# Performance work log

Measured on AMD Instinct MI355X. Metric: run time of the kernel, lower is better.

Reference implementation:

```python
import jax, jax.numpy as jnp
import numpy as np

B, S, N_CATE, N_CONT = 32, 1024, 4, 4
HIDDEN, ATTN, VOCAB, EMB = 1024, 512, 1000, 128


def sinusoidal_pe(seq_len, d_model, base=10000.0):
    pos = jnp.arange(seq_len, dtype=jnp.float32)[:, None]            # [S,1]
    i = jnp.arange(d_model // 2, dtype=jnp.float32)[None, :]         # [1,D/2]
    ang = pos / jnp.power(base, 2.0 * i / d_model)                   # [S,D/2]
    pe = jnp.zeros((seq_len, d_model), dtype=jnp.float32)
    pe = pe.at[:, 0::2].set(jnp.sin(ang))
    pe = pe.at[:, 1::2].set(jnp.cos(ang))
    return pe


def setup_inputs() -> dict:
    key = jax.random.key(0)
    ks = jax.random.split(key, 20)
    s = 0.02
    inp = {
        "cate_x": jax.random.randint(ks[0], (B, S, N_CATE), 0, VOCAB, dtype=jnp.int64)
                  if jax.config.read("jax_enable_x64") else
                  jax.random.randint(ks[0], (B, S, N_CATE), 0, VOCAB, dtype=jnp.int32),
        "cont_x": jax.random.normal(ks[1], (B, S, N_CONT), dtype=jnp.float32),
        "mask": jnp.ones((B, S), dtype=bool),
        "targets": jax.random.uniform(ks[2], (B, S), dtype=jnp.float32),
        # EntireEmbedding params: 4 cate tables + cont linear + comb projection
        "E0": jax.random.normal(ks[3], (VOCAB, EMB), dtype=jnp.float32) * s,
        "E1": jax.random.normal(ks[4], (VOCAB, EMB), dtype=jnp.float32) * s,
        "E2": jax.random.normal(ks[5], (VOCAB, EMB), dtype=jnp.float32) * s,
        "E3": jax.random.normal(ks[6], (VOCAB, EMB), dtype=jnp.float32) * s,
        "Wc": jax.random.normal(ks[7], (N_CONT, N_CATE * EMB), dtype=jnp.float32) * s,
        "Wproj": jax.random.normal(ks[8], (2 * N_CATE * EMB, HIDDEN), dtype=jnp.float32) * s,
        # two-head attention linears (bias=False)
        "WQ1": jax.random.normal(ks[9], (HIDDEN, ATTN), dtype=jnp.float32) * s,
        "WK1": jax.random.normal(ks[10], (HIDDEN, ATTN), dtype=jnp.float32) * s,
        "WV1": jax.random.normal(ks[11], (HIDDEN, ATTN), dtype=jnp.float32) * s,
        "WQ2": jax.random.normal(ks[12], (HIDDEN, ATTN), dtype=jnp.float32) * s,
        "WK2": jax.random.normal(ks[13], (HIDDEN, ATTN), dtype=jnp.float32) * s,
        "WV2": jax.random.normal(ks[14], (HIDDEN, ATTN), dtype=jnp.float32) * s,
        "W0": jax.random.normal(ks[15], (2 * ATTN, HIDDEN), dtype=jnp.float32) * s,
        "Wf": jax.random.normal(ks[16], (HIDDEN, 1), dtype=jnp.float32) * s,
    }
    return inp


def _attend(x, WQ, WK, WV):
    Q = x @ WQ  # [B,S,A]
    K = x @ WK
    V = x @ WV
    scores = jnp.einsum("bqd,bkd->bqk", Q, K) / jnp.sqrt(jnp.float32(ATTN))
    # faithful to nn.Softmax(dim=1): normalize over the QUERY axis
    attn = jax.nn.softmax(scores, axis=1)
    return jnp.einsum("bqk,bkv->bqv", attn, V)


def reference(cate_x, cont_x, mask, targets, E0, E1, E2, E3, Wc, Wproj,
              WQ1, WK1, WV1, WQ2, WK2, WV2, W0, Wf):
    # EntireEmbedding: per-feature cate embeddings + cont projection -> comb proj
    cate_emb = jnp.concatenate(
        [E0[cate_x[..., 0]], E1[cate_x[..., 1]], E2[cate_x[..., 2]], E3[cate_x[..., 3]]],
        axis=-1)                                   # [B,S,512]
    cont_emb = cont_x @ Wc                          # [B,S,512]
    x = jnp.concatenate([cate_emb, cont_emb], axis=-1) @ Wproj  # [B,S,H]
    x = x + sinusoidal_pe(x.shape[1], HIDDEN)[None, :, :]
    z1 = _attend(x, WQ1, WK1, WV1)                  # [B,S,A]
    z2 = _attend(x, WQ2, WK2, WV2)                  # [B,S,A]
    z = jnp.concatenate([z1, z2], axis=-1) @ W0     # [B,S,H]
    out = jax.nn.sigmoid(z @ Wf)                    # FinalConnecting: Linear(H,1)+sigmoid
    return out.squeeze(-1)                          # [B,S]
```

## Files before the change

kernel.cpp:

```cpp
#include <hip/hip_runtime.h>
#include <hip/hip_bf16.h>
#include <math.h>

#define BB    32
#define SS    1024
#define HID   1024
#define AT    512
#define NVOC  1000
#define NT    (BB*SS)

typedef unsigned short u16;
typedef __attribute__((ext_vector_type(8))) short s16x8;
typedef __attribute__((ext_vector_type(4))) float f32x4;

__device__ __forceinline__ float bf2f(u16 u) {
    union { unsigned int i; float f; } x; x.i = ((unsigned int)u) << 16; return x.f;
}
__device__ __forceinline__ u16 f2bf(float f) {
    union { float f; unsigned int i; } u; u.f = f;
    unsigned int r = u.i + 0x7fffu + ((u.i >> 16) & 1u);
    return (u16)(r >> 16);
}
__device__ __forceinline__ float4 ld4(const float* p) { return *(const float4*)p; }
__device__ __forceinline__ float4 ld4bf(const u16* p) {
    ushort4 v = *(const ushort4*)p;
    return make_float4(bf2f(v.x), bf2f(v.y), bf2f(v.z), bf2f(v.w));
}
__device__ __forceinline__ void unpack8(uint4 v, float* x) {
    x[0] = bf2f((u16)(v.x & 0xffff)); x[1] = bf2f((u16)(v.x >> 16));
    x[2] = bf2f((u16)(v.y & 0xffff)); x[3] = bf2f((u16)(v.y >> 16));
    x[4] = bf2f((u16)(v.z & 0xffff)); x[5] = bf2f((u16)(v.z >> 16));
    x[6] = bf2f((u16)(v.w & 0xffff)); x[7] = bf2f((u16)(v.w >> 16));
}

__device__ __forceinline__ void gld16(const u16* g, u16* l) {
    __builtin_amdgcn_global_load_lds(
        (const __attribute__((address_space(1))) unsigned int*)g,
        (__attribute__((address_space(3))) unsigned int*)l,
        16, 0, 0);
}

struct Ptrs4f { const float* p[4]; };

__device__ __forceinline__ float blockReduceSum(float x) {
    #pragma unroll
    for (int off = 32; off > 0; off >>= 1) x += __shfl_down(x, off, 64);
    __shared__ float tmp[4];
    int lane = threadIdx.x & 63, wid = threadIdx.x >> 6;
    if (lane == 0) tmp[wid] = x;
    __syncthreads();
    if (threadIdx.x == 0) x = tmp[0] + tmp[1] + tmp[2] + tmp[3];
    return x;
}
__device__ __forceinline__ float waveReduceSum(float x) {
    #pragma unroll
    for (int off = 32; off > 0; off >>= 1) x += __shfl_down(x, off, 64);
    return x;
}

__global__ void k_s1(Ptrs4f E, const float* __restrict__ Wproj, Ptrs4f W,
                     const float* __restrict__ W0, const float* __restrict__ Wf,
                     u16* __restrict__ PE16, u16* __restrict__ E16o, u16* __restrict__ Wp16,
                     u16* __restrict__ Wt, float* __restrict__ W0f,
                     float* __restrict__ Wcp, float* __restrict__ CQ) {
    int blk = blockIdx.x, tid = threadIdx.x;
    if (blk < 2048) {
        int idx = blk*256 + tid;
        int s = idx >> 9, i = idx & 511;
        const float l2_10000 = 13.287712379549449f;
        float denom = exp2f((2.f * (float)i / 1024.f) * l2_10000);
        float ang = (float)s / denom;
        unsigned int pack = ((unsigned int)f2bf(__cosf(ang)) << 16) | f2bf(__sinf(ang));
        *(unsigned int*)(PE16 + (size_t)s*1024 + 2*i) = pack;
    } else if (blk < 4048) {
        int id2 = blk - 2048;
        int f = id2 / 500;
        int i = (id2 % 500)*256 + tid;
        E16o[(size_t)f*128000 + i] = f2bf(E.p[f][i]);
    } else if (blk < 6096) {
        int i = (blk - 4048)*256 + tid;
        Wp16[i] = f2bf(Wproj[i]);
    } else if (blk < 8144) {
        int tb = blk - 6096;
        int mat = tb >> 9, t2 = tb & 511;
        int cx = t2 & 15, ry = t2 >> 4;
        int r0 = ry*32, c0 = cx*32;
        const float* in = W.p[mat];
        u16* out = Wt + (size_t)mat*1024*512;
        __shared__ float tt[32][33];
        int tx = tid & 31, ty8 = tid >> 5;
        #pragma unroll
        for (int it = 0; it < 4; ++it)
            tt[ty8 + it*8][tx] = in[(size_t)(r0 + ty8 + it*8)*512 + c0 + tx];
        __syncthreads();
        #pragma unroll
        for (int it = 0; it < 4; ++it)
            out[(size_t)(c0 + ty8 + it*8)*1024 + r0 + tx] = f2bf(tt[tx][ty8 + it*8]);
    } else if (blk < 8400) {
        int wave = tid >> 6, lane = tid & 63;
        int row = (blk - 8144)*4 + wave;
        const float* rp = W0 + (size_t)row*1024;
        float a = 0.f;
        #pragma unroll
        for (int i = 0; i < 16; ++i) {
            int j = i*64 + lane;
            a += rp[j] * Wf[j];
        }
        a = waveReduceSum(a);
        if (lane == 0) W0f[row] = a;
    } else {
        int idx = (blk - 8400)*256 + tid;
        if (idx < 4096) Wcp[idx] = 0.f;
        else CQ[idx - 4096] = 0.f;
    }
}

__global__ void k_s2(const float* __restrict__ Wc, const float* __restrict__ Wproj,
                     Ptrs4f W, const float* __restrict__ WV1, const float* __restrict__ WV2,
                     const float* __restrict__ W0f, float* __restrict__ Wcp, float* __restrict__ v) {
    int blk = blockIdx.x, tid = threadIdx.x;
    if (blk < 64) {
        int c = blk >> 4, ic = (blk >> 2) & 3, jc = blk & 3;
        int i = ic*256 + tid;
        float a = 0.f;
        for (int j = jc*128; j < jc*128 + 128; ++j)
            a += Wc[c*512 + j] * Wproj[(size_t)(512 + j)*1024 + i];
        atomicAdd(&Wcp[c*1024 + i], a);
    } else {
        int b2 = blk - 64;
        int h = b2 >> 10, i = b2 & 1023;
        const float* WV = h ? WV2 : WV1;
        const float* wf = W0f + h*512;
        float a = 0.f;
        for (int aa = tid; aa < 512; aa += 256) a += WV[(size_t)i*512 + aa] * wf[aa];
        a = blockReduceSum(a);
        if (tid == 0) v[h*1024 + i] = a;
    }
}

__device__ __forceinline__ void cstore(float* p, float v) { *p = v; }
__device__ __forceinline__ void cstore(u16* p, float v)   { *p = f2bf(v); }

template<typename CT, bool CTRANS>
__device__ __forceinline__ void mfma_gemm(const u16* __restrict__ A, const u16* __restrict__ B,
                                          CT* __restrict__ C, int M, int N, int K, float alpha,
                                          int m0, int n0) {
    __shared__ u16 As[128*64];
    __shared__ u16 Bs[128*64];
    const int tid = threadIdx.x;
    const int wave = tid >> 6, lane = tid & 63;
    const int quad = lane >> 4, l16 = lane & 15;
    const int wm = (wave >> 1)*64, wn = (wave & 1)*64;
    const int srow = lane >> 3;
    const int scol = ((lane & 7) ^ srow) * 8;
    f32x4 acc[4][4] = {};

    for (int k0 = 0; k0 < K; k0 += 64) {
        #pragma unroll
        for (int p = 0; p < 4; ++p) {
            int rb = wave*32 + p*8;
            gld16(A + (size_t)(m0 + rb + srow)*K + k0 + scol, As + rb*64);
            gld16(B + (size_t)(n0 + rb + srow)*K + k0 + scol, Bs + rb*64);
        }
        __syncthreads();
        #pragma unroll
        for (int kk = 0; kk < 2; ++kk) {
            s16x8 af[4], bf[4];
            #pragma unroll
            for (int i = 0; i < 4; ++i) {
                int row = wm + i*16 + l16;
                af[i] = *(const s16x8*)(As + row*64 + (((kk*4 + quad) ^ (row & 7)) * 8));
            }
            #pragma unroll
            for (int j = 0; j < 4; ++j) {
                int row = wn + j*16 + l16;
                bf[j] = *(const s16x8*)(Bs + row*64 + (((kk*4 + quad) ^ (row & 7)) * 8));
            }
            #pragma unroll
            for (int i = 0; i < 4; ++i)
                #pragma unroll
                for (int j = 0; j < 4; ++j)
                    acc[i][j] = __builtin_amdgcn_mfma_f32_16x16x32_bf16(af[i], bf[j], acc[i][j], 0, 0, 0);
        }
        __syncthreads();
    }
    #pragma unroll
    for (int i = 0; i < 4; ++i) {
        #pragma unroll
        for (int r = 0; r < 4; ++r) {
            int gm = m0 + wm + i*16 + quad*4 + r;
            if (gm < M) {
                #pragma unroll
                for (int j = 0; j < 4; ++j) {
                    int gn = n0 + wn + j*16 + l16;
                    if (CTRANS) cstore(C + (size_t)gn*M + gm, acc[i][j][r] * alpha);
                    else        cstore(C + (size_t)gm*N + gn, acc[i][j][r] * alpha);
                }
            }
        }
    }
}

__global__ __launch_bounds__(256) void k_s3(const u16* __restrict__ Wp16, const u16* __restrict__ Wt,
                                            u16* __restrict__ PWT,
                                            const u16* __restrict__ PE16, u16* __restrict__ PEQ16,
                                            Ptrs4f W, const float* __restrict__ Wcp, float* __restrict__ CQ,
                                            const float* __restrict__ Wproj, const float* __restrict__ v,
                                            float* __restrict__ pv) {
    int blk = blockIdx.x, tid = threadIdx.x;
    if (blk < 64) {
        int x = blk & 3, z = blk >> 2;
        int f = z >> 2, w = z & 3;
        mfma_gemm<u16,true>(Wp16 + (size_t)f*128*1024, Wt + (size_t)w*512*1024,
                            PWT + (size_t)z*512*128, 128, 512, 1024, 1.f, 0, x*128);
    } else if (blk < 192) {
        int idx = blk - 64;
        int w = idx >> 5, r2 = idx & 31, y = r2 >> 2, x = r2 & 3;
        mfma_gemm<u16,false>(PE16, Wt + (size_t)w*512*1024, PEQ16 + (size_t)w*1024*512,
                             1024, 512, 1024, 1.f, y*128, x*128);
    } else if (blk < 448) {
        int r = blk - 192;
        int ns = r & 1, wc = (r >> 1) & 15, jc = r >> 5;
        int w = wc & 3, c = wc >> 2; int n = ns*256 + tid;
        const float* Ww = W.p[w];
        float a = 0.f;
        for (int j = jc*128; j < jc*128 + 128; ++j) a += Wcp[c*1024 + j] * Ww[(size_t)j*512 + n];
        atomicAdd(&CQ[(size_t)(w*4 + c)*512 + n], a);
    } else {
        int b2 = blk - 448;
        int i = b2 & 127, fh = b2 >> 7; int f = fh >> 1, h = fh & 1;
        const float* row = Wproj + (size_t)(f*128 + i)*1024;
        const float* vh = v + h*1024;
        float a = 0.f;
        for (int j = tid; j < 1024; j += 256) a += row[j] * vh[j];
        a = blockReduceSum(a);
        if (tid == 0) pv[(size_t)fh*128 + i] = a;
    }
}

__global__ __launch_bounds__(256) void k_s4(const u16* __restrict__ E16, const u16* __restrict__ PWT,
                                            const u16* __restrict__ PE16,
                                            u16* __restrict__ TQK16,
                                            const float* __restrict__ Wcp, const float* __restrict__ v,
                                            const float* __restrict__ pv,
                                            float* __restrict__ Ut, float* __restrict__ pu, float* __restrict__ cu) {
    int blk = blockIdx.x, tid = threadIdx.x;
    int wave = tid >> 6, lane = tid & 63;
    if (blk < 512) {
        int z = blk >> 5, r = blk & 31, y = r >> 2, x = r & 3;
        int f = z >> 2;
        mfma_gemm<u16,false>(E16 + (size_t)f*128000, PWT + (size_t)z*512*128,
                   TQK16 + (size_t)z*1000*512, 1000, 512, 128, 1.f, y*128, x*128);
        return;
    }
    int id = blk - 512;
    if (id < 32) {
        int d = id*256 + tid;
        if (d < 8000) {
            int f = d / 2000, h = (d / 1000) & 1, r = d % 1000;
            const u16* er = E16 + ((size_t)f*1000 + r)*128;
            const float* pvp = pv + (size_t)(f*2 + h)*128;
            float a = 0.f;
            #pragma unroll
            for (int q = 0; q < 16; ++q) {
                float xv[8];
                unpack8(*(const uint4*)(er + q*8), xv);
                #pragma unroll
                for (int e = 0; e < 8; ++e) a += xv[e] * pvp[q*8 + e];
            }
            Ut[(size_t)(f*2 + h)*1000 + r] = a;
        }
    } else if (id < 544) {
        int d = (id - 32)*4 + wave;
        int h = d >> 10, s = d & 1023;
        float a = 0.f;
        #pragma unroll
        for (int half = 0; half < 2; ++half) {
            int k = half*512 + lane*8;
            float xv[8];
            unpack8(*(const uint4*)(PE16 + (size_t)s*1024 + k), xv);
            float4 b0 = ld4(v + h*1024 + k), b1 = ld4(v + h*1024 + k + 4);
            a += xv[0]*b0.x + xv[1]*b0.y + xv[2]*b0.z + xv[3]*b0.w
               + xv[4]*b1.x + xv[5]*b1.y + xv[6]*b1.z + xv[7]*b1.w;
        }
        a = waveReduceSum(a);
        if (lane == 0) pu[h*1024 + s] = a;
    } else {
        #pragma unroll
        for (int rep = 0; rep < 2; ++rep) {
            int d = wave*2 + rep;
            int h = d >> 2, c = d & 3;
            float a = 0.f;
            #pragma unroll
            for (int i = 0; i < 16; ++i) {
                int j = i*64 + lane;
                a += Wcp[c*1024 + j] * v[h*1024 + j];
            }
            a = waveReduceSum(a);
            if (lane == 0) cu[h*4 + c] = a;
        }
    }
}

__global__ __launch_bounds__(512, 2) void k_g_S256(
        const u16* __restrict__ Q, const u16* __restrict__ K,
        u16* __restrict__ Sb, float alpha,
        float* __restrict__ Pm, float* __restrict__ Pd, int b0) {
    __shared__ u16 As[2][16384];
    __shared__ u16 Bs[2][16384];
    const int tid = threadIdx.x;
    const int wave = tid >> 6, lane = tid & 63;
    const int quad = lane >> 4, l16 = lane & 15;
    const int wm = wave >> 2, wn = wave & 3;

    const int nwg = (int)gridDim.x;
    int fblk = (int)blockIdx.x;
    int qq = nwg >> 3, rr = nwg & 7;
    int xcd = fblk & 7, idx = fblk >> 3;
    int swz = (xcd < rr ? xcd*(qq + 1) : rr*(qq + 1) + (xcd - rr)*qq) + idx;
    int b = swz >> 4, tile = swz & 15;
    int m0 = (tile >> 2) << 8, n0 = (tile & 3) << 8;

    const u16* __restrict__ Ab = Q + (size_t)b*SS*AT;
    const u16* __restrict__ Bb = K + (size_t)b*SS*AT;
    u16* __restrict__ C = Sb + (size_t)b*SS*SS;

    const int srow = lane >> 3;
    const int scol = ((lane & 7) ^ srow) * 8;

    f32x4 acc[8][4] = {};

    auto stageA = [&](int kt, int q) {
        gld16(Ab + (size_t)(m0 + q*64 + wave*8 + srow)*AT + kt*64 + scol,
              &As[kt & 1][q*4096 + wave*512]);
    };
    auto stageB = [&](int kt, int q) {
        gld16(Bb + (size_t)(n0 + q*64 + wave*8 + srow)*AT + kt*64 + scol,
              &Bs[kt & 1][q*4096 + wave*512]);
    };

    s16x8 af[4][2];
    s16x8 bf[4][2];

    auto readA = [&](int c, int ih) {
        #pragma unroll
        for (int i2 = 0; i2 < 4; ++i2) {
            int row = wm*128 + (ih*4 + i2)*16 + l16;
            #pragma unroll
            for (int kk = 0; kk < 2; ++kk)
                af[i2][kk] = *(const s16x8*)(&As[c][row*64 + (((kk*4 + quad) ^ (row & 7)) * 8)]);
        }
    };
    auto readB2 = [&](int c, int jh) {
        #pragma unroll
        for (int j2 = 0; j2 < 2; ++j2) {
            int j = jh*2 + j2;
            int row = wn*64 + j*16 + l16;
            #pragma unroll
            for (int kk = 0; kk < 2; ++kk)
                bf[j][kk] = *(const s16x8*)(&Bs[c][row*64 + (((kk*4 + quad) ^ (row & 7)) * 8)]);
        }
    };
    auto mma16 = [&](int ih, int jh) {
        __builtin_amdgcn_s_setprio(1);
        #pragma unroll
        for (int i2 = 0; i2 < 4; ++i2)
            #pragma unroll
            for (int j2 = 0; j2 < 2; ++j2) {
                int i = ih*4 + i2, j = jh*2 + j2;
                acc[i][j] = __builtin_amdgcn_mfma_f32_16x16x32_bf16(af[i2][0], bf[j][0], acc[i][j], 0, 0, 0);
                acc[i][j] = __builtin_amdgcn_mfma_f32_16x16x32_bf16(af[i2][1], bf[j][1], acc[i][j], 0, 0, 0);
            }
        __builtin_amdgcn_s_setprio(0);
    };
    auto midsync = [&]() {
        __builtin_amdgcn_s_barrier();
        asm volatile("s_waitcnt lgkmcnt(0)" ::: "memory");
        __builtin_amdgcn_sched_barrier(0);
    };

    #pragma unroll
    for (int q = 0; q < 4; ++q) stageA(0, q);
    #pragma unroll
    for (int q = 0; q < 4; ++q) stageB(0, q);
    stageA(1, 0); stageA(1, 2);
    stageB(1, 0); stageB(1, 1); stageB(1, 2); stageB(1, 3);
    asm volatile("s_waitcnt vmcnt(6)" ::: "memory");
    __builtin_amdgcn_s_barrier();

    #pragma unroll
    for (int t = 0; t < 8; ++t) {
        const int c = t & 1;
        readA(c, 0);
        readB2(c, 0);
        if (t <= 6) { stageA(t + 1, 1); stageA(t + 1, 3); }
        midsync();
        mma16(0, 0);
        __builtin_amdgcn_s_barrier();
        readB2(c, 1);
        if (t <= 5) { stageA(t + 2, 0); stageA(t + 2, 2); }
        midsync();
        mma16(0, 1);
        __builtin_amdgcn_s_barrier();
        readA(c, 1);
        if (t <= 5) { stageB(t + 2, 0); stageB(t + 2, 1); }
        midsync();
        mma16(1, 0);
        __builtin_amdgcn_s_barrier();
        if (t <= 5) { stageB(t + 2, 2); stageB(t + 2, 3); }
        midsync();
        mma16(1, 1);
        if (t <= 5)      asm volatile("s_waitcnt vmcnt(6)" ::: "memory");
        else if (t == 6) asm volatile("s_waitcnt vmcnt(0)" ::: "memory");
        __builtin_amdgcn_sched_barrier(0);
        __builtin_amdgcn_s_barrier();
    }

    #pragma unroll
    for (int i = 0; i < 8; ++i) {
        #pragma unroll
        for (int r = 0; r < 4; ++r) {
            int gm = m0 + wm*128 + i*16 + quad*4 + r;
            u16 q0 = f2bf(acc[i][0][r] * alpha);
            u16 q1 = f2bf(acc[i][1][r] * alpha);
            u16 q2 = f2bf(acc[i][2][r] * alpha);
            u16 q3 = f2bf(acc[i][3][r] * alpha);
            acc[i][0][r] = bf2f(q0); acc[i][1][r] = bf2f(q1);
            acc[i][2][r] = bf2f(q2); acc[i][3][r] = bf2f(q3);
            unsigned int lo = (unsigned int)q0 | ((unsigned int)q1 << 16);
            unsigned int hi = (unsigned int)q2 | ((unsigned int)q3 << 16);
            *(uint2*)(C + (size_t)gm*SS + n0 + wn*64 + l16*4) = make_uint2(lo, hi);
        }
    }
    float* sM = (float*)&As[0][0];
    float* sS = (float*)&Bs[0][0];
    #pragma unroll
    for (int j = 0; j < 4; ++j) {
        float mx = -3.4e38f;
        #pragma unroll
        for (int i = 0; i < 8; ++i)
            #pragma unroll
            for (int r = 0; r < 4; ++r) mx = fmaxf(mx, acc[i][j][r]);
        mx = fmaxf(mx, __shfl_xor(mx, 16, 64));
        mx = fmaxf(mx, __shfl_xor(mx, 32, 64));
        float sm = 0.f;
        #pragma unroll
        for (int i = 0; i < 8; ++i)
            #pragma unroll
            for (int r = 0; r < 4; ++r) sm += exp2f(acc[i][j][r] - mx);
        sm += __shfl_xor(sm, 16, 64);
        sm += __shfl_xor(sm, 32, 64);
        if (quad == 0) { sM[wave*64 + j*16 + l16] = mx; sS[wave*64 + j*16 + l16] = sm; }
    }
    __syncthreads();
    if (tid < 256) {
        int c = tid, wq = c >> 6, cc = c & 63;
        float ma = sM[wq*64 + cc],       sa = sS[wq*64 + cc];
        float mb = sM[(4 + wq)*64 + cc], sb2 = sS[(4 + wq)*64 + cc];
        float mm = fmaxf(ma, mb);
        float ss = sa * exp2f(ma - mm) + sb2 * exp2f(mb - mm);
        size_t po = ((size_t)(b0 + b)*4 + (m0 >> 8))*1024;
        Pm[po + n0 + c] = mm;
        Pd[po + n0 + c] = ss;
    }
}

__global__ __launch_bounds__(256) void k_gather(
                         const int* __restrict__ cate, const float* __restrict__ cont,
                         const u16* __restrict__ TQK, const float* __restrict__ CQ,
                         const u16* __restrict__ PEQ, const float* __restrict__ Ut,
                         const float* __restrict__ cu, const float* __restrict__ pu,
                         u16* __restrict__ Qh, u16* __restrict__ Kh,
                         float* __restrict__ u, int h) {
    int tid = threadIdx.x;
    int g = blockIdx.x & 7;
    size_t t = (size_t)(blockIdx.x >> 3)*32 + (tid >> 3);
    int cslot = tid & 7;
    int s = (int)(t & 1023);
    int4 cc = *(const int4*)(cate + t*4);
    float4 cv = ld4(cont + t*4);
    int n = g*64 + cslot*8;
    #pragma unroll
    for (int e = 0; e < 2; ++e) {
        int w = 2*h + e;
        const u16* t0 = TQK + ((size_t)(0*4  + w)*1000 + cc.x)*512 + n;
        const u16* t1 = TQK + ((size_t)(1*4  + w)*1000 + cc.y)*512 + n;
        const u16* t2 = TQK + ((size_t)(2*4  + w)*1000 + cc.z)*512 + n;
        const u16* t3 = TQK + ((size_t)(3*4  + w)*1000 + cc.w)*512 + n;
        const u16* pq = PEQ + ((size_t)w*1024 + s)*512 + n;
        const float* cq = CQ + (size_t)w*2048 + n;
        float a0[8], a1[8], a2[8], a3[8], ap[8];
        unpack8(*(const uint4*)t0, a0); unpack8(*(const uint4*)t1, a1);
        unpack8(*(const uint4*)t2, a2); unpack8(*(const uint4*)t3, a3);
        unpack8(*(const uint4*)pq, ap);
        unsigned int pack[4];
        #pragma unroll
        for (int jp = 0; jp < 4; ++jp) {
            float x0, x1;
            #pragma unroll
            for (int half = 0; half < 2; ++half) {
                int j = jp*2 + half;
                float x = a0[j] + a1[j] + a2[j] + a3[j] + ap[j]
                        + cv.x*cq[j] + cv.y*cq[512+j] + cv.z*cq[1024+j] + cv.w*cq[1536+j];
                if (half == 0) x0 = x; else x1 = x;
            }
            pack[jp] = ((unsigned int)f2bf(x1) << 16) | f2bf(x0);
        }
        u16* op = (e ? Kh : Qh) + t*512 + n;
        *(uint4*)op = make_uint4(pack[0], pack[1], pack[2], pack[3]);
    }
    if (g == 0 && (tid & 7) == 0) {
        float uu = pu[h*1024 + s]
                 + Ut[(0*2 + h)*1000 + cc.x] + Ut[(1*2 + h)*1000 + cc.y]
                 + Ut[(2*2 + h)*1000 + cc.z] + Ut[(3*2 + h)*1000 + cc.w]
                 + cv.x*cu[h*4+0] + cv.y*cu[h*4+1] + cv.z*cu[h*4+2] + cv.w*cu[h*4+3];
        u[(size_t)h*NT + t] = uu;
    }
}

__global__ __launch_bounds__(1024) void k_logit(const u16* __restrict__ Sb,
                        const float* __restrict__ Pm, const float* __restrict__ Pd,
                        const float* __restrict__ u,
                        float* __restrict__ logits, float* __restrict__ out,
                        int b0, int mode) {
    __shared__ float wsm[1024];
    int wave = threadIdx.x >> 6, lane = threadIdx.x & 63;
    size_t bi = (size_t)(gridDim.x - 1 - blockIdx.x);
    size_t tl0 = bi*16;
    size_t tabs0 = (size_t)b0*1024 + tl0;
    int ab = (int)(tabs0 >> 10);
    {
        int k = threadIdx.x;
        float mx = -3.4e38f;
        #pragma unroll
        for (int mt = 0; mt < 4; ++mt) mx = fmaxf(mx, Pm[((size_t)ab*4 + mt)*1024 + k]);
        float dd = 0.f;
        #pragma unroll
        for (int mt = 0; mt < 4; ++mt) dd += Pd[((size_t)ab*4 + mt)*1024 + k]
                                           * exp2f(Pm[((size_t)ab*4 + mt)*1024 + k] - mx);
        int q = (k & ~63) | (((k & 15) << 2) | ((k & 63) >> 4));
        wsm[q] = u[(size_t)ab*1024 + k] / dd * exp2f(-mx);
    }
    __syncthreads();
    size_t tl = tl0 + wave;
    size_t tabs = tabs0 + wave;
    const u16* row = Sb + tl*1024;
    float acc = 0.f;
    #pragma unroll
    for (int half = 0; half < 2; ++half) {
        int k = lane*8 + half*512;
        float sv[8];
        unpack8(*(const uint4*)(row + k), sv);
        float4 w0 = ld4(wsm + k), w1 = ld4(wsm + k + 4);
        acc += exp2f(sv[0])*w0.x + exp2f(sv[1])*w0.y + exp2f(sv[2])*w0.z + exp2f(sv[3])*w0.w
             + exp2f(sv[4])*w1.x + exp2f(sv[5])*w1.y + exp2f(sv[6])*w1.z + exp2f(sv[7])*w1.w;
    }
    acc = waveReduceSum(acc);
    if (lane == 0) {
        if (mode == 0) logits[tabs] = acc;
        else {
            float x = logits[tabs] + acc;
            out[tabs] = 1.f / (1.f + expf(-x));
        }
    }
}

extern "C" void kernel_launch(void* const* d_in, const int* in_sizes, int n_in,
                              void* d_out, int out_size, void* d_ws, size_t ws_size,
                              hipStream_t stream) {
    const int*   cate = (const int*)d_in[0];
    const float* cont = (const float*)d_in[1];
    Ptrs4f E; E.p[0] = (const float*)d_in[4]; E.p[1] = (const float*)d_in[5];
              E.p[2] = (const float*)d_in[6]; E.p[3] = (const float*)d_in[7];
    const float* Wc    = (const float*)d_in[8];
    const float* Wproj = (const float*)d_in[9];
    Ptrs4f W; W.p[0] = (const float*)d_in[10];
              W.p[1] = (const float*)d_in[11];
              W.p[2] = (const float*)d_in[13];
              W.p[3] = (const float*)d_in[14];
    const float* WV1 = (const float*)d_in[12];
    const float* WV2 = (const float*)d_in[15];
    const float* W0  = (const float*)d_in[16];
    const float* Wf  = (const float*)d_in[17];

    char* base = (char*)d_ws;
    size_t off = 0;
    auto alloc = [&](size_t bytes) { void* p = base + off; off += (bytes + 255) & ~(size_t)255; return p; };
    u16*   PE16  = (u16*)  alloc(1048576ull*2);
    u16*   E16   = (u16*)  alloc(4ull*1000*128*2);
    u16*   Wt    = (u16*)  alloc(4ull*512*1024*2);
    u16*   Wp16  = (u16*)  alloc(512ull*1024*2);
    u16*   PWT   = (u16*)  alloc(16ull*512*128*2);
    u16*   TQK16 = (u16*)  alloc(16ull*1000*512*2);
    u16*   PEQ16 = (u16*)  alloc(4ull*1024*512*2);
    float* Wcp   = (float*)alloc(4*1024*4);
    float* W0f   = (float*)alloc(1024*4);
    float* vv    = (float*)alloc(2*1024*4);
    float* CQ    = (float*)alloc(16*512*4);
    float* pvb   = (float*)alloc(8*128*4);
    float* Ut    = (float*)alloc(8*1000*4);
    float* cu    = (float*)alloc(8*4);
    float* pu    = (float*)alloc(2*1024*4);
    float* ubuf  = (float*)alloc(2ull*NT*4);
    u16*   Qh    = (u16*)  alloc((size_t)NT*512*2);
    u16*   Kh    = (u16*)  alloc((size_t)NT*512*2);
    float* Pm    = (float*)alloc(32ull*8*1024*4);
    float* Pd    = (float*)alloc(32ull*8*1024*4);
    float* logits= (float*)alloc((size_t)NT*4);
    size_t sChunkBytes = (size_t)SS*SS*2;
    size_t remain = (ws_size > off) ? (ws_size - off) : 0;
    int NB = (int)(remain / sChunkBytes);
    if (NB > 32) NB = 32;
    if (NB < 1) NB = 1;
    u16* Sbuf = (u16*)(base + off);

    const float alpha = 0.06375954951107036f;

    k_s1<<<8448, 256, 0, stream>>>(E, Wproj, W, W0, Wf, PE16, E16, Wp16, Wt, W0f, Wcp, CQ);
    k_s2<<<2112, 256, 0, stream>>>(Wc, Wproj, W, WV1, WV2, W0f, Wcp, vv);
    k_s3<<<1472, 256, 0, stream>>>(Wp16, Wt, PWT, PE16, PEQ16, W, Wcp, CQ, Wproj, vv, pvb);
    k_s4<<<1057, 256, 0, stream>>>(E16, PWT, PE16, TQK16, Wcp, vv, pvb, Ut, pu, cu);

    for (int h = 0; h < 2; ++h) {
        k_gather<<<8192, 256, 0, stream>>>(cate, cont, TQK16, CQ, PEQ16, Ut, cu, pu, Qh, Kh, ubuf, h);
        for (int b0 = 0; b0 < 32; b0 += NB) {
            int nb = (32 - b0 < NB) ? (32 - b0) : NB;
            k_g_S256<<<16*nb, 512, 0, stream>>>(Qh + (size_t)b0*SS*AT, Kh + (size_t)b0*SS*AT,
                                                Sbuf, alpha, Pm, Pd, b0);
            k_logit<<<nb*64, 1024, 0, stream>>>(Sbuf, Pm, Pd, ubuf + (size_t)h*NT,
                                                logits, (float*)d_out, b0, h);
        }
    }
}
```

Baseline: 339.1 us.

## Compute two N-tiles per workgroup with continuous pipeline across tiles

Each QK^T GEMM workgroup now computes two adjacent 256x256 score tiles, running a single 16-step loop whose prefetch carries straight from the first tile into the second, with the epilogue (bf16 store plus column max/sum partials) emitted in the middle and at the end. This halves the grid and hides the pipeline ramp-up and drain of the second tile, at the cost of less parallelism (256 workgroups per chunk) and dedicated shared memory for the partials. Separately, k_logit's shared weight array is transposed to [8][128] so that lanes read consecutive addresses, avoiding bank conflicts from the float4 loads.

```diff
diff --git a/kernel.cpp b/kernel.cpp
--- a/kernel.cpp
+++ b/kernel.cpp
@@ -308,6 +308,8 @@
         float* __restrict__ Pm, float* __restrict__ Pd, int b0) {
     __shared__ u16 As[2][16384];
     __shared__ u16 Bs[2][16384];
+    __shared__ float sM[8][64];
+    __shared__ float sS[8][64];
     const int tid = threadIdx.x;
     const int wave = tid >> 6, lane = tid & 63;
     const int quad = lane >> 4, l16 = lane & 15;
@@ -318,8 +320,9 @@
     int qq = nwg >> 3, rr = nwg & 7;
     int xcd = fblk & 7, idx = fblk >> 3;
     int swz = (xcd < rr ? xcd*(qq + 1) : rr*(qq + 1) + (xcd - rr)*qq) + idx;
-    int b = swz >> 4, tile = swz & 15;
-    int m0 = (tile >> 2) << 8, n0 = (tile & 3) << 8;
+    int b = swz >> 3, tile = swz & 7;
+    int m0 = (tile >> 1) << 8;
+    int nbase = (tile & 1) << 9;
 
     const u16* __restrict__ Ab = Q + (size_t)b*SS*AT;
     const u16* __restrict__ Bb = K + (size_t)b*SS*AT;
@@ -330,13 +333,16 @@
 
     f32x4 acc[8][4] = {};
 
-    auto stageA = [&](int kt, int q) {
+    auto stageA = [&](int t, int q) {
+        int kt = t & 7;
         gld16(Ab + (size_t)(m0 + q*64 + wave*8 + srow)*AT + kt*64 + scol,
-              &As[kt & 1][q*4096 + wave*512]);
+              &As[t & 1][q*4096 + wave*512]);
     };
-    auto stageB = [&](int kt, int q) {
-        gld16(Bb + (size_t)(n0 + q*64 + wave*8 + srow)*AT + kt*64 + scol,
-              &Bs[kt & 1][q*4096 + wave*512]);
+    auto stageB = [&](int t, int q) {
+        int kt = t & 7;
+        int nn = nbase + ((t >> 3) << 8);
+        gld16(Bb + (size_t)(nn + q*64 + wave*8 + srow)*AT + kt*64 + scol,
+              &Bs[t & 1][q*4096 + wave*512]);
     };
 
     s16x8 af[4][2];
@@ -377,6 +383,55 @@
         __builtin_amdgcn_s_barrier();
         asm volatile("s_waitcnt lgkmcnt(0)" ::: "memory");
         __builtin_amdgcn_sched_barrier(0);
+    };
+
+    auto epilogue = [&](int half) {
+        int n0h = nbase + half*256;
+        #pragma unroll
+        for (int i = 0; i < 8; ++i) {
+            #pragma unroll
+            for (int r = 0; r < 4; ++r) {
+                int gm = m0 + wm*128 + i*16 + quad*4 + r;
+                u16 q0 = f2bf(acc[i][0][r] * alpha);
+                u16 q1 = f2bf(acc[i][1][r] * alpha);
+                u16 q2 = f2bf(acc[i][2][r] * alpha);
+                u16 q3 = f2bf(acc[i][3][r] * alpha);
+                acc[i][0][r] = bf2f(q0); acc[i][1][r] = bf2f(q1);
+                acc[i][2][r] = bf2f(q2); acc[i][3][r] = bf2f(q3);
+                unsigned int lo = (unsigned int)q0 | ((unsigned int)q1 << 16);
+                unsigned int hi = (unsigned int)q2 | ((unsigned int)q3 << 16);
+                *(uint2*)(C + (size_t)gm*SS + n0h + wn*64 + l16*4) = make_uint2(lo, hi);
+            }
+        }
+        #pragma unroll
+        for (int j = 0; j < 4; ++j) {
+            float mx = -3.4e38f;
+            #pragma unroll
+            for (int i = 0; i < 8; ++i)
+                #pragma unroll
+                for (int r = 0; r < 4; ++r) mx = fmaxf(mx, acc[i][j][r]);
+            mx = fmaxf(mx, __shfl_xor(mx, 16, 64));
+            mx = fmaxf(mx, __shfl_xor(mx, 32, 64));
+            float sm = 0.f;
+            #pragma unroll
+            for (int i = 0; i < 8; ++i)
+                #pragma unroll
+                for (int r = 0; r < 4; ++r) sm += exp2f(acc[i][j][r] - mx);
+            sm += __shfl_xor(sm, 16, 64);
+            sm += __shfl_xor(sm, 32, 64);
+            if (quad == 0) { sM[wave][j*16 + l16] = mx; sS[wave][j*16 + l16] = sm; }
+        }
+        __syncthreads();
+        if (tid < 256) {
+            int c = tid, wq = c >> 6, cc = c & 63;
+            float ma = sM[wq][cc],     sa = sS[wq][cc];
+            float mb = sM[4 + wq][cc], sb2 = sS[4 + wq][cc];
+            float mm = fmaxf(ma, mb);
+            float ss = sa * exp2f(ma - mm) + sb2 * exp2f(mb - mm);
+            size_t po = ((size_t)(b0 + b)*4 + (m0 >> 8))*1024;
+            Pm[po + n0h + c] = mm;
+            Pd[po + n0h + c] = ss;
+        }
     };
 
     #pragma unroll
@@ -388,80 +443,45 @@
     asm volatile("s_waitcnt vmcnt(6)" ::: "memory");
     __builtin_amdgcn_s_barrier();
 
-    #pragma unroll
-    for (int t = 0; t < 8; ++t) {
+    #pragma unroll 2
+    for (int t = 0; t < 16; ++t) {
         const int c = t & 1;
         readA(c, 0);
         readB2(c, 0);
-        if (t <= 6) { stageA(t + 1, 1); stageA(t + 1, 3); }
+        if (t <= 14) { stageA(t + 1, 1); stageA(t + 1, 3); }
         midsync();
         mma16(0, 0);
         __builtin_amdgcn_s_barrier();
         readB2(c, 1);
-        if (t <= 5) { stageA(t + 2, 0); stageA(t + 2, 2); }
+        if (t <= 13) { stageA(t + 2, 0); stageA(t + 2, 2); }
         midsync();
         mma16(0, 1);
         __builtin_amdgcn_s_barrier();
         readA(c, 1);
-        if (t <= 5) { stageB(t + 2, 0); stageB(t + 2, 1); }
+        if (t <= 13) { stageB(t + 2, 0); stageB(t + 2, 1); }
         midsync();
         mma16(1, 0);
         __builtin_amdgcn_s_barrier();
-        if (t <= 5) { stageB(t + 2, 2); stageB(t + 2, 3); }
+        if (t <= 13) { stageB(t + 2, 2); stageB(t + 2, 3); }
         midsync();
         mma16(1, 1);
-        if (t <= 5)      asm volatile("s_waitcnt vmcnt(6)" ::: "memory");
-        else if (t == 6) asm volatile("s_waitcnt vmcnt(0)" ::: "memory");
+        if (t <= 13)      asm volatile("s_waitcnt vmcnt(6)" ::: "memory");
+        else if (t == 14) asm volatile("s_waitcnt vmcnt(0)" ::: "memory");
         __builtin_amdgcn_sched_barrier(0);
         __builtin_amdgcn_s_barrier();
-    }
-
-    #pragma unroll
-    for (int i = 0; i < 8; ++i) {
-        #pragma unroll
-        for (int r = 0; r < 4; ++r) {
-            int gm = m0 + wm*128 + i*16 + quad*4 + r;
-            u16 q0 = f2bf(acc[i][0][r] * alpha);
-            u16 q1 = f2bf(acc[i][1][r] * alpha);
-            u16 q2 = f2bf(acc[i][2][r] * alpha);
-            u16 q3 = f2bf(acc[i][3][r] * alpha);
-            acc[i][0][r] = bf2f(q0); acc[i][1][r] = bf2f(q1);
-            acc[i][2][r] = bf2f(q2); acc[i][3][r] = bf2f(q3);
-            unsigned int lo = (unsigned int)q0 | ((unsigned int)q1 << 16);
-            unsigned int hi = (unsigned int)q2 | ((unsigned int)q3 << 16);
-            *(uint2*)(C + (size_t)gm*SS + n0 + wn*64 + l16*4) = make_uint2(lo, hi);
-        }
-    }
-    float* sM = (float*)&As[0][0];
-    float* sS = (float*)&Bs[0][0];
-    #pragma unroll
-    for (int j = 0; j < 4; ++j) {
-        float mx = -3.4e38f;
-        #pragma unroll
-        for (int i = 0; i < 8; ++i)
-            #pragma unroll
-            for (int r = 0; r < 4; ++r) mx = fmaxf(mx, acc[i][j][r]);
-        mx = fmaxf(mx, __shfl_xor(mx, 16, 64));
-        mx = fmaxf(mx, __shfl_xor(mx, 32, 64));
-        float sm = 0.f;
-        #pragma unroll
-        for (int i = 0; i < 8; ++i)
-            #pragma unroll
-            for (int r = 0; r < 4; ++r) sm += exp2f(acc[i][j][r] - mx);
-        sm += __shfl_xor(sm, 16, 64);
-        sm += __shfl_xor(sm, 32, 64);
-        if (quad == 0) { sM[wave*64 + j*16 + l16] = mx; sS[wave*64 + j*16 + l16] = sm; }
-    }
-    __syncthreads();
-    if (tid < 256) {
-        int c = tid, wq = c >> 6, cc = c & 63;
-        float ma = sM[wq*64 + cc],       sa = sS[wq*64 + cc];
-        float mb = sM[(4 + wq)*64 + cc], sb2 = sS[(4 + wq)*64 + cc];
-        float mm = fmaxf(ma, mb);
-        float ss = sa * exp2f(ma - mm) + sb2 * exp2f(mb - mm);
-        size_t po = ((size_t)(b0 + b)*4 + (m0 >> 8))*1024;
-        Pm[po + n0 + c] = mm;
-        Pd[po + n0 + c] = ss;
+
+        if ((t & 7) == 7) {
+            epilogue(t >> 3);
+            if (t == 7) {
+                #pragma unroll
+                for (int i = 0; i < 8; ++i)
+                    #pragma unroll
+                    for (int j = 0; j < 4; ++j)
+                        #pragma unroll
+                        for (int r = 0; r < 4; ++r) acc[i][j][r] = 0.f;
+                __syncthreads();
+            }
+        }
     }
 }
 
@@ -523,7 +543,7 @@
                         const float* __restrict__ u,
                         float* __restrict__ logits, float* __restrict__ out,
                         int b0, int mode) {
-    __shared__ float wsm[1024];
+    __shared__ float wsm[8][128];
     int wave = threadIdx.x >> 6, lane = threadIdx.x & 63;
     size_t bi = (size_t)(gridDim.x - 1 - blockIdx.x);
     size_t tl0 = bi*16;
@@ -539,7 +559,7 @@
         for (int mt = 0; mt < 4; ++mt) dd += Pd[((size_t)ab*4 + mt)*1024 + k]
                                            * exp2f(Pm[((size_t)ab*4 + mt)*1024 + k] - mx);
         int q = (k & ~63) | (((k & 15) << 2) | ((k & 63) >> 4));
-        wsm[q] = u[(size_t)ab*1024 + k] / dd * exp2f(-mx);
+        wsm[q & 7][q >> 3] = u[(size_t)ab*1024 + k] / dd * exp2f(-mx);
     }
     __syncthreads();
     size_t tl = tl0 + wave;
@@ -549,11 +569,13 @@
     #pragma unroll
     for (int half = 0; half < 2; ++half) {
         int k = lane*8 + half*512;
+        int li = lane + half*64;
         float sv[8];
         unpack8(*(const uint4*)(row + k), sv);
-        float4 w0 = ld4(wsm + k), w1 = ld4(wsm + k + 4);
-        acc += exp2f(sv[0])*w0.x + exp2f(sv[1])*w0.y + exp2f(sv[2])*w0.z + exp2f(sv[3])*w0.w
-             + exp2f(sv[4])*w1.x + exp2f(sv[5])*w1.y + exp2f(sv[6])*w1.z + exp2f(sv[7])*w1.w;
+        acc += exp2f(sv[0])*wsm[0][li] + exp2f(sv[1])*wsm[1][li]
+             + exp2f(sv[2])*wsm[2][li] + exp2f(sv[3])*wsm[3][li]
+             + exp2f(sv[4])*wsm[4][li] + exp2f(sv[5])*wsm[5][li]
+             + exp2f(sv[6])*wsm[6][li] + exp2f(sv[7])*wsm[7][li];
     }
     acc = waveReduceSum(acc);
     if (lane == 0) {
@@ -625,8 +647,8 @@
         k_gather<<<8192, 256, 0, stream>>>(cate, cont, TQK16, CQ, PEQ16, Ut, cu, pu, Qh, Kh, ubuf, h);
         for (int b0 = 0; b0 < 32; b0 += NB) {
             int nb = (32 - b0 < NB) ? (32 - b0) : NB;
-            k_g_S256<<<16*nb, 512, 0, stream>>>(Qh + (size_t)b0*SS*AT, Kh + (size_t)b0*SS*AT,
-                                                Sbuf, alpha, Pm, Pd, b0);
+            k_g_S256<<<8*nb, 512, 0, stream>>>(Qh + (size_t)b0*SS*AT, Kh + (size_t)b0*SS*AT,
+                                               Sbuf, alpha, Pm, Pd, b0);
             k_logit<<<nb*64, 1024, 0, stream>>>(Sbuf, Pm, Pd, ubuf + (size_t)h*NT,
                                                 logits, (float*)d_out, b0, h);
         }
```

New measurement: 357.3 us. +5.4%, slower.
